# Kernel optimization log

Hardware: AMD Instinct MI355X
Metric: run time of the kernel (lower is better)

Reference implementation:

```python
import jax, jax.numpy as jnp
import numpy as np

# norse default LIFParameters
DT = 1e-3
TAU_SYN_INV = 200.0
TAU_MEM_INV = 100.0
V_LEAK = 0.0
V_TH = 1.0
V_RESET = 0.0


def heaviside(x):
    return (x > 0).astype(x.dtype)


def setup_inputs() -> dict:
    key = jax.random.key(0)
    ks = jax.random.split(key, 5)
    T, B, I, H, O = 14, 4096, 2048, 1024, 128
    x = (jax.random.uniform(ks[0], (T, B, I), dtype=jnp.float32) < 0.2).astype(jnp.float32)  # spike train
    w_in = jax.random.normal(ks[1], (H, I), dtype=jnp.float32) * (1.0 / np.sqrt(I))
    w_rec = jax.random.normal(ks[2], (H, H), dtype=jnp.float32) * (1.0 / np.sqrt(H))
    out_w = jax.random.normal(ks[3], (O, H), dtype=jnp.float32) * (1.0 / np.sqrt(H))
    out_b = jax.random.normal(ks[4], (O,), dtype=jnp.float32) * 0.01
    return {"x": x, "w_in": w_in, "w_rec": w_rec, "out_w": out_w, "out_b": out_b}


def reference(x, w_in, w_rec, out_w, out_b):
    T, B, _ = x.shape
    H = w_in.shape[0]
    z0 = jnp.zeros((B, H), dtype=x.dtype)
    v0 = jnp.full((B, H), V_LEAK, dtype=x.dtype)
    i0 = jnp.zeros((B, H), dtype=x.dtype)

    def step(carry, x_t):
        z, v, i = carry
        v_dec = v + DT * TAU_MEM_INV * ((V_LEAK - v) + i)   # membrane integration
        i_dec = i - DT * TAU_SYN_INV * i                    # synaptic decay
        z_new = heaviside(v_dec - V_TH)                     # spike
        v_new = (1.0 - z_new) * v_dec + z_new * V_RESET     # reset
        i_new = i_dec + x_t @ w_in.T + z @ w_rec.T          # input + recurrent current
        return (z_new, v_new, i_new), None

    (z_T, _, _), _ = jax.lax.scan(step, (z0, v0, i0), x)
    return z_T @ out_w.T + out_b
```

## Files before the change

### kernel.cpp

```cpp
#include <hip/hip_runtime.h>
#include <hip/hip_cooperative_groups.h>
#include <stdint.h>

namespace cg = cooperative_groups;

#define T_STEPS 14
#define B_DIM   4096
#define I_DIM   2048
#define H_DIM   1024
#define O_DIM   128
#define K_TOT   3072

#define WSCALE_F 33554432.0f

typedef __bf16  bf16x8  __attribute__((ext_vector_type(8)));
typedef float   floatx4 __attribute__((ext_vector_type(4)));
typedef int     int4v   __attribute__((ext_vector_type(4)));
typedef int     int16v  __attribute__((ext_vector_type(16)));

__device__ __forceinline__ uint16_t f2bf_rne(float f) {
    uint32_t u = __float_as_uint(f);
    u += 0x7fffu + ((u >> 16) & 1u);
    return (uint16_t)(u >> 16);
}
__device__ __forceinline__ float bf2f(uint16_t h) {
    return __uint_as_float(((uint32_t)h) << 16);
}

__device__ __forceinline__ void gload_lds16(const void* g, void* l) {
    __builtin_amdgcn_global_load_lds((__attribute__((address_space(1))) void*)g,
                                     (__attribute__((address_space(3))) void*)l, 16, 0, 0);
}


__global__ void split_w_kernel(const float* __restrict__ w_in, const float* __restrict__ w_rec,
                               int8_t* __restrict__ WB) {
    int idx = blockIdx.x * 256 + threadIdx.x;
    int h = idx / K_TOT;
    int k = idx - h * K_TOT;
    float w = (k < I_DIM) ? w_in[(size_t)h * I_DIM + k]
                          : w_rec[(size_t)h * H_DIM + (k - I_DIM)];
    int W  = __float2int_rn(w * WSCALE_F);
    int d0 = (int8_t)(W & 0xFF);
    int r1 = (W - d0) >> 8;
    int d1 = (int8_t)(r1 & 0xFF);
    int d2 = (r1 - d1) >> 8;
    int nt = h >> 5, n32 = h & 31;
    int ktw = k >> 7, k128 = k & 127;
    int kk = k128 >> 5, half = (k128 >> 4) & 1, j = k128 & 15;
    int lane = half * 32 + n32;
    size_t base = (size_t)(nt * 24 + ktw) * 12288 + kk * 1024 + lane * 16 + j;
    WB[base] = (int8_t)d0; WB[base + 4096] = (int8_t)d1; WB[base + 8192] = (int8_t)d2;
}

__global__ void split_ow_kernel(const float* __restrict__ out_w, uint16_t* __restrict__ OW3) {
    int idx = blockIdx.x * 256 + threadIdx.x;
    float w = out_w[idx];
    uint16_t hi = f2bf_rne(w);
    float r1 = w - bf2f(hi);
    uint16_t mid = f2bf_rne(r1);
    float r2 = r1 - bf2f(mid);
    uint16_t lo = f2bf_rne(r2);
    const size_t S = (size_t)O_DIM * H_DIM;
    OW3[idx] = hi; OW3[idx + S] = mid; OW3[idx + 2 * S] = lo;
}

__global__ void cvt_x_kernel(const float* __restrict__ x, int8_t* __restrict__ xb) {
    size_t gid = (size_t)blockIdx.x * 256 + threadIdx.x;
    int g = (int)(gid & 1023);
    size_t chunk = gid >> 10;
    int kt   = (int)(chunk & 15);
    int mIdx = (int)((chunk >> 4) & 31);
    int t    = (int)(chunk >> 9);
    int group = g >> 8, kk = (g >> 6) & 3, lane = g & 63;
    int half = lane >> 5, row32 = lane & 31;
    int b = mIdx * 128 + group * 32 + row32;
    int k = kt * 128 + kk * 32 + half * 16;
    const float4* src = (const float4*)(x + ((size_t)t * B_DIM + b) * I_DIM + k);
    union { int8_t bytes[16]; int4v v; } u;
#pragma unroll
    for (int q = 0; q < 4; ++q) {
        float4 f = src[q];
        u.bytes[q * 4 + 0] = (int8_t)(f.x > 0.5f);
        u.bytes[q * 4 + 1] = (int8_t)(f.y > 0.5f);
        u.bytes[q * 4 + 2] = (int8_t)(f.z > 0.5f);
        u.bytes[q * 4 + 3] = (int8_t)(f.w > 0.5f);
    }
    ((int4v*)xb)[gid] = u.v;
}

__launch_bounds__(256, 4)
__global__ void lif_persist_kernel(const int8_t* __restrict__ Xall,
                                   const int8_t* __restrict__ WB,
                                   int8_t* __restrict__ Z0,
                                   int8_t* __restrict__ Z1,
                                   uint16_t* __restrict__ Zbf) {
    __shared__ int8_t sA[16384];
    __shared__ int8_t sB[12288];

    const int tid  = threadIdx.x;
    const int wave = tid >> 6, lane = tid & 63;
    const int lane32 = lane & 31, hl = lane >> 5;

    const int nt = blockIdx.x & 31, mIdx = blockIdx.x >> 5;
    const int mBase = mIdx * 128, nBase = nt * 32;

    float vmem[16], isyn[16];
#pragma unroll
    for (int r = 0; r < 16; ++r) { vmem[r] = 0.0f; isyn[r] = 0.0f; }

    int8_t* zA = Z0;
    int8_t* zB = Z1;

    for (int t = 0; t < T_STEPS; ++t) {
        int16v acc[3] = {};
        const int8_t* Xt = Xall + (size_t)t * ((size_t)B_DIM * I_DIM);

        for (int kt = 0; kt < 16; ++kt) {
            __syncthreads();
            const int8_t* chunkA = Xt + ((size_t)mIdx * 16 + kt) * 16384;
#pragma unroll
            for (int j = 0; j < 4; ++j) {
                const int seg = j * 4 + wave;
                gload_lds16(chunkA + seg * 1024 + lane * 16, &sA[seg * 1024]);
            }
            const int8_t* chunkB = WB + (size_t)(nt * 24 + kt) * 12288;
#pragma unroll
            for (int j = 0; j < 3; ++j) {
                const int seg = j * 4 + wave;
                gload_lds16(chunkB + seg * 1024 + lane * 16, &sB[seg * 1024]);
            }
            __syncthreads();
#pragma unroll
            for (int kk = 0; kk < 4; ++kk) {
                int4v aF = *(const int4v*)&sA[wave * 4096 + kk * 1024 + lane * 16];
#pragma unroll
                for (int s = 0; s < 3; ++s) {
                    int4v bF = *(const int4v*)&sB[s * 4096 + kk * 1024 + lane * 16];
                    acc[s] = __builtin_amdgcn_mfma_i32_32x32x32_i8(aF, bF, acc[s], 0, 0, 0);
                }
            }
        }

        if (t > 0) {
            cg::this_grid().sync();
            for (int kt = 0; kt < 8; ++kt) {
                __syncthreads();
                const int8_t* chunkA = zA + ((size_t)mIdx * 8 + kt) * 16384;
#pragma unroll
                for (int j = 0; j < 4; ++j) {
                    const int seg = j * 4 + wave;
                    gload_lds16(chunkA + seg * 1024 + lane * 16, &sA[seg * 1024]);
                }
                const int8_t* chunkB = WB + (size_t)(nt * 24 + 16 + kt) * 12288;
#pragma unroll
                for (int j = 0; j < 3; ++j) {
                    const int seg = j * 4 + wave;
                    gload_lds16(chunkB + seg * 1024 + lane * 16, &sB[seg * 1024]);
                }
                __syncthreads();
#pragma unroll
                for (int kk = 0; kk < 4; ++kk) {
                    int4v aF = *(const int4v*)&sA[wave * 4096 + kk * 1024 + lane * 16];
#pragma unroll
                    for (int s = 0; s < 3; ++s) {
                        int4v bF = *(const int4v*)&sB[s * 4096 + kk * 1024 + lane * 16];
                        acc[s] = __builtin_amdgcn_mfma_i32_32x32x32_i8(aF, bF, acc[s], 0, 0, 0);
                    }
                }
            }
        }

        int8_t* zchunk = zB + ((size_t)mIdx * 8 + (nt >> 2)) * 16384;
#pragma unroll
        for (int r = 0; r < 16; ++r) {
#pragma clang fp contract(off)
            float cur = (float)acc[2][r] * (1.0f / 512.0f)
                      + (float)acc[1][r] * (1.0f / 131072.0f)
                      + (float)acc[0][r] * (1.0f / 33554432.0f);
            int row = (r & 3) + 8 * (r >> 2) + 4 * hl;
            float v_dec = vmem[r] + 0.1f * ((0.0f - vmem[r]) + isyn[r]);
            float i_dec = isyn[r] - 0.2f * isyn[r];
            bool z = (v_dec > 1.0f);
            vmem[r] = z ? 0.0f : v_dec;
            isyn[r] = i_dec + cur;
            if (t == T_STEPS - 1) {
                int b = mBase + wave * 32 + row;
                int h = nBase + lane32;
                Zbf[(size_t)b * H_DIM + h] = z ? (uint16_t)0x3F80 : (uint16_t)0;
            } else {
                zchunk[wave * 4096 + (nt & 3) * 1024
                       + ((lane32 >> 4) * 32 + row) * 16 + (lane32 & 15)]
                    = z ? (int8_t)1 : (int8_t)0;
            }
        }

        int8_t* tmp = zA; zA = zB; zB = tmp;
    }
}

__launch_bounds__(256, 4)
__global__ void lif_step_kernel(const int8_t* __restrict__ Xt,
                                const int8_t* __restrict__ Zin,
                                const int8_t* __restrict__ WB,
                                float2* __restrict__ VI,
                                int8_t* __restrict__ Zout,
                                uint16_t* __restrict__ Zbf, int t) {
    __shared__ int8_t sA[16384];
    __shared__ int8_t sB[12288];

    const int tid  = threadIdx.x;
    const int wave = tid >> 6, lane = tid & 63;
    const int lane32 = lane & 31, hl = lane >> 5;

    const int nt = blockIdx.x & 31, mIdx = blockIdx.x >> 5;
    const int mBase = mIdx * 128, nBase = nt * 32;

    int16v acc[3] = {};

    const int nIters = (t > 0) ? 24 : 16;

    for (int kt = 0; kt < nIters; ++kt) {
        __syncthreads();
        const int8_t* chunkA = (kt < 16)
            ? Xt  + ((size_t)mIdx * 16 + kt) * 16384
            : Zin + ((size_t)mIdx * 8 + (kt - 16)) * 16384;
#pragma unroll
        for (int j = 0; j < 4; ++j) {
            const int seg = j * 4 + wave;
            gload_lds16(chunkA + seg * 1024 + lane * 16, &sA[seg * 1024]);
        }
        const int8_t* chunkB = WB + (size_t)(nt * 24 + kt) * 12288;
#pragma unroll
        for (int j = 0; j < 3; ++j) {
            const int seg = j * 4 + wave;
            gload_lds16(chunkB + seg * 1024 + lane * 16, &sB[seg * 1024]);
        }
        __syncthreads();
#pragma unroll
        for (int kk = 0; kk < 4; ++kk) {
            int4v aF = *(const int4v*)&sA[wave * 4096 + kk * 1024 + lane * 16];
#pragma unroll
            for (int s = 0; s < 3; ++s) {
                int4v bF = *(const int4v*)&sB[s * 4096 + kk * 1024 + lane * 16];
                acc[s] = __builtin_amdgcn_mfma_i32_32x32x32_i8(aF, bF, acc[s], 0, 0, 0);
            }
        }
    }

    int8_t* zchunk = Zout + ((size_t)mIdx * 8 + (nt >> 2)) * 16384;
#pragma unroll
    for (int r = 0; r < 16; ++r) {
#pragma clang fp contract(off)
        float cur = (float)acc[2][r] * (1.0f / 512.0f)
                  + (float)acc[1][r] * (1.0f / 131072.0f)
                  + (float)acc[0][r] * (1.0f / 33554432.0f);
        int row = (r & 3) + 8 * (r >> 2) + 4 * hl;
        int b = mBase + wave * 32 + row;
        int h = nBase + lane32;
        size_t idx = (size_t)b * H_DIM + h;
        float v, ii;
        if (t == 0) { v = 0.0f; ii = 0.0f; }
        else        { float2 vi = VI[idx]; v = vi.x; ii = vi.y; }
        float v_dec = v + 0.1f * ((0.0f - v) + ii);
        float i_dec = ii - 0.2f * ii;
        bool z = (v_dec > 1.0f);
        float2 vi_new;
        vi_new.x = z ? 0.0f : v_dec;
        vi_new.y = i_dec + cur;
        VI[idx] = vi_new;
        if (t == T_STEPS - 1) {
            Zbf[idx] = z ? (uint16_t)0x3F80 : (uint16_t)0;
        } else {
            zchunk[wave * 4096 + (nt & 3) * 1024
                   + ((lane32 >> 4) * 32 + row) * 16 + (lane32 & 15)]
                = z ? (int8_t)1 : (int8_t)0;
        }
    }
}

__launch_bounds__(256)
__global__ void out_gemm_kernel(const uint16_t* __restrict__ Zfin,
                                const uint16_t* __restrict__ OW3,
                                const float* __restrict__ out_b,
                                float* __restrict__ out) {
    __shared__ uint16_t sA[16 * 32];
    __shared__ uint16_t sB[3][128 * 32];

    const int tid  = threadIdx.x;
    const int wave = tid >> 6, lane = tid & 63;
    const int quad = lane >> 4, col = lane & 15;

    const int mBase = blockIdx.x * 16;

    floatx4 acc[2] = {};

    const int ldRow = lane >> 2;
    const int ldCol = (lane & 3) * 8;

    for (int kt = 0; kt < H_DIM / 32; ++kt) {
        const int kb = kt * 32;
        __syncthreads();
        if (wave == 0) {
            const uint16_t* g = Zfin + (size_t)(mBase + ldRow) * H_DIM + kb + ldCol;
            gload_lds16(g, &sA[0]);
        }
#pragma unroll
        for (int s = 0; s < 3; ++s) {
            const uint16_t* wsrc = OW3 + (size_t)s * O_DIM * H_DIM;
#pragma unroll
            for (int j = 0; j < 2; ++j) {
                const int rseg = j * 4 + wave;
                const uint16_t* g = wsrc + (size_t)(rseg * 16 + ldRow) * H_DIM + kb + ldCol;
                gload_lds16(g, &sB[s][rseg * 16 * 32]);
            }
        }
        __syncthreads();

        bf16x8 aF = *reinterpret_cast<const bf16x8*>(&sA[col * 32 + quad * 8]);
#pragma unroll
        for (int s = 0; s < 3; ++s) {
#pragma unroll
            for (int ni = 0; ni < 2; ++ni) {
                int row = wave * 32 + ni * 16 + col;
                bf16x8 bF = *reinterpret_cast<const bf16x8*>(&sB[s][row * 32 + quad * 8]);
                acc[ni] = __builtin_amdgcn_mfma_f32_16x16x32_bf16(aF, bF, acc[ni], 0, 0, 0);
            }
        }
    }

    {
#pragma clang fp contract(off)
#pragma unroll
        for (int ni = 0; ni < 2; ++ni)
#pragma unroll
            for (int r = 0; r < 4; ++r) {
                int b = mBase + quad * 4 + r;
                int h = wave * 32 + ni * 16 + col;
                out[(size_t)b * O_DIM + h] = acc[ni][r] + out_b[h];
            }
    }
}

extern "C" void kernel_launch(void* const* d_in, const int* in_sizes, int n_in,
                              void* d_out, int out_size, void* d_ws, size_t ws_size,
                              hipStream_t stream) {
    const float* x     = (const float*)d_in[0];
    const float* w_in  = (const float*)d_in[1];
    const float* w_rec = (const float*)d_in[2];
    const float* out_w = (const float*)d_in[3];
    const float* out_b = (const float*)d_in[4];
    float* out = (float*)d_out;

    char* ws = (char*)d_ws;
    size_t off = 0;
    int8_t*   WB   = (int8_t*)(ws + off);   off += (size_t)3 * H_DIM * K_TOT;
    uint16_t* OW3  = (uint16_t*)(ws + off); off += (size_t)3 * O_DIM * H_DIM * 2;
    int8_t*   Xall = (int8_t*)(ws + off);   off += (size_t)T_STEPS * B_DIM * I_DIM;
    uint16_t* Zbf  = (uint16_t*)(ws + off); off += (size_t)B_DIM * H_DIM * 2;
    int8_t*   Z0   = (int8_t*)(ws + off);   off += (size_t)B_DIM * H_DIM;
    int8_t*   Z1   = (int8_t*)(ws + off);   off += (size_t)B_DIM * H_DIM;
    float2*   VI   = (float2*)(ws + off);   off += (size_t)B_DIM * H_DIM * 8;

    split_w_kernel<<<(H_DIM * K_TOT) / 256, 256, 0, stream>>>(w_in, w_rec, WB);
    split_ow_kernel<<<(O_DIM * H_DIM) / 256, 256, 0, stream>>>(out_w, OW3);
    cvt_x_kernel<<<(int)(((size_t)T_STEPS * B_DIM * I_DIM / 16) / 256), 256, 0, stream>>>(x, Xall);

    static int coop_ok = -1;
    if (coop_ok < 0) {
        int dev = 0, v = 0;
        (void)hipGetDevice(&dev);
        if (hipDeviceGetAttribute(&v, hipDeviceAttributeCooperativeLaunch, dev) != hipSuccess) v = 0;
        coop_ok = v;
    }

    bool launched = false;
    if (coop_ok) {
        void* args[] = { (void*)&Xall, (void*)&WB, (void*)&Z0, (void*)&Z1, (void*)&Zbf };
        hipError_t e = hipLaunchCooperativeKernel((const void*)lif_persist_kernel,
                                                  dim3(1024), dim3(256), args, 0, stream);
        if (e == hipSuccess) launched = true;
        else coop_ok = 0;
    }
    if (!launched) {
        int8_t* zbuf[2] = { Z0, Z1 };
        for (int t = 0; t < T_STEPS; ++t) {
            lif_step_kernel<<<dim3(1024), 256, 0, stream>>>(
                Xall + (size_t)t * B_DIM * I_DIM, zbuf[t & 1], WB, VI,
                zbuf[(t + 1) & 1], Zbf, t);
        }
    }

    out_gemm_kernel<<<B_DIM / 16, 256, 0, stream>>>(Zbf, OW3, out_b, out);
}
```

Baseline: 1.349 ms.

## Double-buffer weight tiles in LDS and load activations directly into registers

The persistent LIF GEMM loop no longer stages the A operand (spikes) through shared memory. Each wave now loads its A fragments straight from global memory into registers. The B (weight) tiles are double-buffered in LDS, and the next chunk is prefetched asynchronously while the current one feeds MFMAs, using manual vmcnt waits and raw s_barriers. This is meant to hide global-to-LDS latency and to halve the number of barriers per k-step. In exchange it relies on hand-tuned waitcnt counts, and A loads with direct global access may coalesce worse.

```diff
diff --git a/kernel.cpp b/kernel.cpp
--- a/kernel.cpp
+++ b/kernel.cpp
@@ -89,14 +89,65 @@
     ((int4v*)xb)[gid] = u.v;
 }
 
+__device__ __forceinline__ void lif_iter(const int8_t* __restrict__ aP,
+                                         const int8_t* __restrict__ bPn,
+                                         const int8_t* cur, int8_t* nxt,
+                                         int wave, int lane, bool stage_next,
+                                         int16v (&acc)[3]) {
+    int4v a0 = *(const int4v*)(aP);
+    int4v a1 = *(const int4v*)(aP + 1024);
+    int4v a2 = *(const int4v*)(aP + 2048);
+    int4v a3 = *(const int4v*)(aP + 3072);
+    __builtin_amdgcn_sched_barrier(0);
+    if (stage_next) {
+        gload_lds16(bPn + (size_t)wave * 1024 + lane * 16,       nxt + wave * 1024);
+        gload_lds16(bPn + (size_t)(4 + wave) * 1024 + lane * 16, nxt + (4 + wave) * 1024);
+        gload_lds16(bPn + (size_t)(8 + wave) * 1024 + lane * 16, nxt + (8 + wave) * 1024);
+        asm volatile("s_waitcnt vmcnt(7)" ::: "memory");
+    } else {
+        asm volatile("s_waitcnt vmcnt(4)" ::: "memory");
+    }
+    __builtin_amdgcn_s_barrier();
+    __builtin_amdgcn_sched_barrier(0);
+#pragma unroll
+    for (int kk = 0; kk < 4; ++kk) {
+        int4v aF = (kk == 0) ? a0 : (kk == 1) ? a1 : (kk == 2) ? a2 : a3;
+#pragma unroll
+        for (int s = 0; s < 3; ++s) {
+            int4v bF = *(const int4v*)(cur + s * 4096 + kk * 1024 + lane * 16);
+            acc[s] = __builtin_amdgcn_mfma_i32_32x32x32_i8(aF, bF, acc[s], 0, 0, 0);
+        }
+    }
+    asm volatile("s_waitcnt lgkmcnt(0)" ::: "memory");
+    __builtin_amdgcn_s_barrier();
+}
+
+template<int NKT>
+__device__ __forceinline__ void run_phase(const int8_t* __restrict__ aChunk0,
+                                          const int8_t* __restrict__ bChunk0,
+                                          int8_t* sB0, int8_t* sB1,
+                                          int wave, int lane, int16v (&acc)[3]) {
+    gload_lds16(bChunk0 + (size_t)wave * 1024 + lane * 16,       sB0 + wave * 1024);
+    gload_lds16(bChunk0 + (size_t)(4 + wave) * 1024 + lane * 16, sB0 + (4 + wave) * 1024);
+    gload_lds16(bChunk0 + (size_t)(8 + wave) * 1024 + lane * 16, sB0 + (8 + wave) * 1024);
+    const int8_t* aW = aChunk0 + wave * 4096 + lane * 16;
+#pragma unroll 1
+    for (int kt = 0; kt + 2 < NKT; kt += 2) {
+        lif_iter(aW + (size_t)kt * 16384,       bChunk0 + (size_t)(kt + 1) * 12288, sB0, sB1, wave, lane, true, acc);
+        lif_iter(aW + (size_t)(kt + 1) * 16384, bChunk0 + (size_t)(kt + 2) * 12288, sB1, sB0, wave, lane, true, acc);
+    }
+    lif_iter(aW + (size_t)(NKT - 2) * 16384, bChunk0 + (size_t)(NKT - 1) * 12288, sB0, sB1, wave, lane, true, acc);
+    lif_iter(aW + (size_t)(NKT - 1) * 16384, nullptr,                             sB1, sB0, wave, lane, false, acc);
+}
+
 __launch_bounds__(256, 4)
 __global__ void lif_persist_kernel(const int8_t* __restrict__ Xall,
                                    const int8_t* __restrict__ WB,
                                    int8_t* __restrict__ Z0,
                                    int8_t* __restrict__ Z1,
                                    uint16_t* __restrict__ Zbf) {
-    __shared__ int8_t sA[16384];
-    __shared__ int8_t sB[12288];
+    __shared__ int8_t sB0[12288];
+    __shared__ int8_t sB1[12288];
 
     const int tid  = threadIdx.x;
     const int wave = tid >> 6, lane = tid & 63;
@@ -104,6 +155,7 @@
 
     const int nt = blockIdx.x & 31, mIdx = blockIdx.x >> 5;
     const int mBase = mIdx * 128, nBase = nt * 32;
+    const int8_t* wbStrip = WB + (size_t)nt * 24 * 12288;
 
     float vmem[16], isyn[16];
 #pragma unroll
@@ -114,61 +166,14 @@
 
     for (int t = 0; t < T_STEPS; ++t) {
         int16v acc[3] = {};
-        const int8_t* Xt = Xall + (size_t)t * ((size_t)B_DIM * I_DIM);
-
-        for (int kt = 0; kt < 16; ++kt) {
-            __syncthreads();
-            const int8_t* chunkA = Xt + ((size_t)mIdx * 16 + kt) * 16384;
-#pragma unroll
-            for (int j = 0; j < 4; ++j) {
-                const int seg = j * 4 + wave;
-                gload_lds16(chunkA + seg * 1024 + lane * 16, &sA[seg * 1024]);
-            }
-            const int8_t* chunkB = WB + (size_t)(nt * 24 + kt) * 12288;
-#pragma unroll
-            for (int j = 0; j < 3; ++j) {
-                const int seg = j * 4 + wave;
-                gload_lds16(chunkB + seg * 1024 + lane * 16, &sB[seg * 1024]);
-            }
-            __syncthreads();
-#pragma unroll
-            for (int kk = 0; kk < 4; ++kk) {
-                int4v aF = *(const int4v*)&sA[wave * 4096 + kk * 1024 + lane * 16];
-#pragma unroll
-                for (int s = 0; s < 3; ++s) {
-                    int4v bF = *(const int4v*)&sB[s * 4096 + kk * 1024 + lane * 16];
-                    acc[s] = __builtin_amdgcn_mfma_i32_32x32x32_i8(aF, bF, acc[s], 0, 0, 0);
-                }
-            }
-        }
+
+        const int8_t* Xt = Xall + (size_t)t * ((size_t)B_DIM * I_DIM) + (size_t)mIdx * 16 * 16384;
+        run_phase<16>(Xt, wbStrip, sB0, sB1, wave, lane, acc);
 
         if (t > 0) {
             cg::this_grid().sync();
-            for (int kt = 0; kt < 8; ++kt) {
-                __syncthreads();
-                const int8_t* chunkA = zA + ((size_t)mIdx * 8 + kt) * 16384;
-#pragma unroll
-                for (int j = 0; j < 4; ++j) {
-                    const int seg = j * 4 + wave;
-                    gload_lds16(chunkA + seg * 1024 + lane * 16, &sA[seg * 1024]);
-                }
-                const int8_t* chunkB = WB + (size_t)(nt * 24 + 16 + kt) * 12288;
-#pragma unroll
-                for (int j = 0; j < 3; ++j) {
-                    const int seg = j * 4 + wave;
-                    gload_lds16(chunkB + seg * 1024 + lane * 16, &sB[seg * 1024]);
-                }
-                __syncthreads();
-#pragma unroll
-                for (int kk = 0; kk < 4; ++kk) {
-                    int4v aF = *(const int4v*)&sA[wave * 4096 + kk * 1024 + lane * 16];
-#pragma unroll
-                    for (int s = 0; s < 3; ++s) {
-                        int4v bF = *(const int4v*)&sB[s * 4096 + kk * 1024 + lane * 16];
-                        acc[s] = __builtin_amdgcn_mfma_i32_32x32x32_i8(aF, bF, acc[s], 0, 0, 0);
-                    }
-                }
-            }
+            run_phase<8>(zA + (size_t)mIdx * 8 * 16384, wbStrip + (size_t)16 * 12288,
+                         sB0, sB1, wave, lane, acc);
         }
 
         int8_t* zchunk = zB + ((size_t)mIdx * 8 + (nt >> 2)) * 16384;
```

Result: no change. 1.350 ms (+0.1%).
